# Kernel optimization log

Hardware: AMD Instinct MI355X
Metric: run time of the kernel (lower is better)

The kernel has to match this reference:

```python
import jax, jax.numpy as jnp
import numpy as np

B, T, C = 4, 2048, 768
N_HEAD = 12
HEAD_DIM = C // N_HEAD


def setup_inputs() -> dict:
    key = jax.random.key(0)
    k1, k2, k3 = jax.random.split(key, 3)
    x = jax.random.normal(k1, (B, T, C), dtype=jnp.float32)
    w_attn = jax.random.normal(k2, (C, 3 * C), dtype=jnp.float32) * (1.0 / np.sqrt(C))
    b_attn = jnp.zeros((3 * C,), dtype=jnp.float32)
    w_proj = jax.random.normal(k3, (C, C), dtype=jnp.float32) * (1.0 / np.sqrt(C))
    b_proj = jnp.zeros((C,), dtype=jnp.float32)
    return {"x": x, "w_attn": w_attn, "b_attn": b_attn, "w_proj": w_proj, "b_proj": b_proj}


def reference(x, w_attn, b_attn, w_proj, b_proj):
    # x: [B, T, C]
    Bs, Ts, Cs = x.shape
    qkv = x @ w_attn + b_attn                         # [B, T, 3C]
    q, k, v = jnp.split(qkv, 3, axis=-1)
    # -> [B, H, T, Dh]
    q = q.reshape(Bs, Ts, N_HEAD, HEAD_DIM).swapaxes(1, 2)
    k = k.reshape(Bs, Ts, N_HEAD, HEAD_DIM).swapaxes(1, 2)
    v = v.reshape(Bs, Ts, N_HEAD, HEAD_DIM).swapaxes(1, 2)
    scale = 1.0 / jnp.sqrt(jnp.asarray(HEAD_DIM, dtype=x.dtype))
    att = jnp.einsum('bhqd,bhkd->bhqk', q, k) * scale  # [B, H, T, T]
    causal = jnp.tril(jnp.ones((Ts, Ts), dtype=bool))[None, None]
    att = jnp.where(causal, att, jnp.asarray(-jnp.inf, dtype=att.dtype))
    att = jax.nn.softmax(att, axis=-1)
    y = jnp.einsum('bhqk,bhkd->bhqd', att, v)          # [B, H, T, Dh]
    y = y.swapaxes(1, 2).reshape(Bs, Ts, Cs)
    y = y @ w_proj + b_proj
    return y
```

## Files before the change

kernel.cpp:

```cpp
#include <hip/hip_runtime.h>
#include <cstdint>
#include <cstddef>

typedef __bf16 bf16x8 __attribute__((ext_vector_type(8)));
typedef float  f32x4  __attribute__((ext_vector_type(4)));
typedef unsigned short us;

#define DEV static __device__ __forceinline__

DEV us f2bf(float f) {
    unsigned int u = __builtin_bit_cast(unsigned int, f);
    u += 0x7FFFu + ((u >> 16) & 1u);
    return (us)(u >> 16);
}
DEV unsigned int pack2bf(float a, float b) {
    unsigned int ua = __builtin_bit_cast(unsigned int, a) + 0x8000u;
    unsigned int ub = __builtin_bit_cast(unsigned int, b) + 0x8000u;
    return (ua >> 16) | (ub & 0xFFFF0000u);
}

DEV void gll16(const void* g, void* l) {
    __builtin_amdgcn_global_load_lds(
        (const __attribute__((address_space(1))) unsigned int*)g,
        (__attribute__((address_space(3))) unsigned int*)l, 16, 0, 0);
}

DEV bf16x8 ld_frag(const us* p) {
    return __builtin_bit_cast(bf16x8, *reinterpret_cast<const uint4*>(p));
}

#define BB 4
#define TT 2048
#define CC 768
#define NH 12
#define DH 64
#define MM (BB*TT)
#define QSCALE 0.1803368801111144f

__global__ __launch_bounds__(256)
void cast_k(const float* __restrict__ x, us* __restrict__ xb, int n4)
{
    int i = blockIdx.x * 256 + threadIdx.x;
    int stride = gridDim.x * 256;
    for (; i < n4; i += stride) {
        float4 f = reinterpret_cast<const float4*>(x)[i];
        ushort4 o;
        o.x = f2bf(f.x); o.y = f2bf(f.y); o.z = f2bf(f.z); o.w = f2bf(f.w);
        reinterpret_cast<ushort4*>(xb)[i] = o;
    }
}

__global__ __launch_bounds__(256)
void transpose_k(const float* __restrict__ src,
                 us* __restrict__ dst, int R, int Cc)
{
    __shared__ float tile[32][33];
    int c0 = blockIdx.x * 32, r0 = blockIdx.y * 32;
    int tx = threadIdx.x, ty = threadIdx.y;
#pragma unroll
    for (int i = 0; i < 4; ++i)
        tile[ty + i*8][tx] = src[(size_t)(r0 + ty + i*8) * Cc + c0 + tx];
    __syncthreads();
#pragma unroll
    for (int i = 0; i < 4; ++i)
        dst[(size_t)(c0 + ty + i*8) * R + r0 + tx] = f2bf(tile[tx][ty + i*8]);
}

#define BM 128
#define BN 128
#define BK 32

template<int MODE>
__global__ __launch_bounds__(256)
void gemm_bt(const us* __restrict__ A,
             const us* __restrict__ Bt,
             const float* __restrict__ bias,
             float* __restrict__ Cout,
             us* __restrict__ Qo, us* __restrict__ Ko, us* __restrict__ Vo,
             int M, int N, int K)
{
    __shared__ __align__(16) us As[BM * BK];
    __shared__ __align__(16) us Bs[BN * BK];

    const int tid  = threadIdx.x;
    const int wave = tid >> 6, lane = tid & 63;
    const int quad = lane >> 4, l16 = lane & 15;
    const int waveM = (wave >> 1) * 64, waveN = (wave & 1) * 64;
    const int m0 = blockIdx.y * BM, n0 = blockIdx.x * BN;

    const f32x4 zero4 = {0.f, 0.f, 0.f, 0.f};
    f32x4 acc[4][4];
#pragma unroll
    for (int i = 0; i < 4; ++i)
#pragma unroll
        for (int j = 0; j < 4; ++j) acc[i][j] = zero4;

    const int lrow = lane >> 2, lch = (lane & 3) * 8;
    const int nk = K / BK;
    for (int kt = 0; kt < nk; ++kt) {
#pragma unroll
        for (int c = 0; c < 2; ++c) {
            int rb = (wave * 2 + c) * 16;
            int row = rb + lrow;
            gll16(A  + (size_t)(m0 + row) * K + kt * BK + lch, &As[rb * BK]);
            gll16(Bt + (size_t)(n0 + row) * K + kt * BK + lch, &Bs[rb * BK]);
        }
        __syncthreads();

        bf16x8 af[4], bfv[4];
#pragma unroll
        for (int mi = 0; mi < 4; ++mi)
            af[mi] = *reinterpret_cast<const bf16x8*>(&As[(waveM + mi * 16 + l16) * BK + quad * 8]);
#pragma unroll
        for (int ni = 0; ni < 4; ++ni)
            bfv[ni] = *reinterpret_cast<const bf16x8*>(&Bs[(waveN + ni * 16 + l16) * BK + quad * 8]);
#pragma unroll
        for (int mi = 0; mi < 4; ++mi)
#pragma unroll
            for (int ni = 0; ni < 4; ++ni)
                acc[mi][ni] = __builtin_amdgcn_mfma_f32_16x16x32_bf16(af[mi], bfv[ni], acc[mi][ni], 0, 0, 0);
        __syncthreads();
    }

#pragma unroll
    for (int mi = 0; mi < 4; ++mi) {
#pragma unroll
        for (int ni = 0; ni < 4; ++ni) {
            int n = n0 + waveN + ni * 16 + l16;
            float bv = bias[n];
            int mg = m0 + waveM + mi * 16 + quad * 4;
            if (MODE == 0) {
#pragma unroll
                for (int reg = 0; reg < 4; ++reg)
                    Cout[(size_t)(mg + reg) * N + n] = acc[mi][ni][reg] + bv;
            } else {
                int which = n / CC, c2 = n % CC;
                int h = c2 >> 6, d = c2 & 63;
                int b = mg >> 11, t0 = mg & 2047;
                if (which == 2) {
                    ushort4 pk;
                    pk.x = f2bf(acc[mi][ni][0] + bv);
                    pk.y = f2bf(acc[mi][ni][1] + bv);
                    pk.z = f2bf(acc[mi][ni][2] + bv);
                    pk.w = f2bf(acc[mi][ni][3] + bv);
                    *reinterpret_cast<ushort4*>(Vo + ((size_t)(b * NH + h) * DH + d) * TT + t0) = pk;
                } else {
#pragma unroll
                    for (int reg = 0; reg < 4; ++reg) {
                        size_t off = ((size_t)(b * NH + h) * TT + t0 + reg) * DH + d;
                        float v = acc[mi][ni][reg] + bv;
                        if (which == 0) Qo[off] = f2bf(v * QSCALE);
                        else            Ko[off] = f2bf(v);
                    }
                }
            }
        }
    }
}

#define PST 72

__global__ __launch_bounds__(128)
void attn_k(const us* __restrict__ Qg,
            const us* __restrict__ Kg,
            const us* __restrict__ Vt,
            us* __restrict__ Og)
{
    __shared__ __align__(16) us Ps[2][32 * PST];

    const int tid  = threadIdx.x;
    const int wave = tid >> 6, lane = tid & 63;
    const int quad = lane >> 4, l16 = lane & 15;

    const int id  = blockIdx.x;
    const int xcd = id & 7, s = id >> 3;
    const int bh  = xcd + 8 * (s >> 4);
    const int q   = s & 15;
    const int pw  = 2 * q + wave;

    const size_t base  = (size_t)bh * TT * DH;
    const size_t baseV = (size_t)bh * DH * TT;
    const int b = bh / NH, h = bh % NH;
    us* myP = Ps[wave];

    const f32x4 zero4 = {0.f, 0.f, 0.f, 0.f};

#pragma unroll 1
    for (int seg = 0; seg < 2; ++seg) {
        const int g   = seg ? 63 - pw : pw;
        const int nkt = (g >> 1) + 1;
        const int mA  = g * 32 + l16;
        const int mB  = mA + 16;

        bf16x8 qfA0 = ld_frag(Qg + base + (size_t)mA * DH + quad * 8);
        bf16x8 qfA1 = ld_frag(Qg + base + (size_t)mA * DH + 32 + quad * 8);
        bf16x8 qfB0 = ld_frag(Qg + base + (size_t)mB * DH + quad * 8);
        bf16x8 qfB1 = ld_frag(Qg + base + (size_t)mB * DH + 32 + quad * 8);

        f32x4 oA[4], oB[4];
#pragma unroll
        for (int i = 0; i < 4; ++i) { oA[i] = zero4; oB[i] = zero4; }
        float mrA = -INFINITY, lrA = 0.f, mrB = -INFINITY, lrB = 0.f;

#pragma unroll 1
        for (int j = 0; j < nkt; ++j) {
            const us* kb = Kg + base  + (size_t)j * 64 * DH;
            const us* vb = Vt + baseV + j * 64;

            bf16x8 kf[4][2];
#pragma unroll
            for (int sub = 0; sub < 4; ++sub)
#pragma unroll
                for (int hh = 0; hh < 2; ++hh)
                    kf[sub][hh] = ld_frag(kb + (size_t)(sub * 16 + l16) * DH + hh * 32 + quad * 8);

            f32x4 sA[4], sB[4];
#pragma unroll
            for (int sub = 0; sub < 4; ++sub) {
                f32x4 t = __builtin_amdgcn_mfma_f32_16x16x32_bf16(kf[sub][0], qfA0, zero4, 0, 0, 0);
                sA[sub]  = __builtin_amdgcn_mfma_f32_16x16x32_bf16(kf[sub][1], qfA1, t, 0, 0, 0);
                f32x4 u = __builtin_amdgcn_mfma_f32_16x16x32_bf16(kf[sub][0], qfB0, zero4, 0, 0, 0);
                sB[sub]  = __builtin_amdgcn_mfma_f32_16x16x32_bf16(kf[sub][1], qfB1, u, 0, 0, 0);
            }

            bf16x8 vf[4][2];
#pragma unroll
            for (int dsub = 0; dsub < 4; ++dsub)
#pragma unroll
                for (int kc = 0; kc < 2; ++kc)
                    vf[dsub][kc] = ld_frag(vb + (size_t)(dsub * 16 + l16) * TT + kc * 32 + quad * 8);

            if (j == nkt - 1) {
#pragma unroll
                for (int sub = 0; sub < 4; ++sub)
#pragma unroll
                    for (int reg = 0; reg < 4; ++reg) {
                        int key = j * 64 + sub * 16 + quad * 4 + reg;
                        if (key > mA) sA[sub][reg] = -INFINITY;
                        if (key > mB) sB[sub][reg] = -INFINITY;
                    }
            }

            {
                float mx = -INFINITY;
#pragma unroll
                for (int sub = 0; sub < 4; ++sub)
#pragma unroll
                    for (int reg = 0; reg < 4; ++reg) mx = fmaxf(mx, sA[sub][reg]);
                mx = fmaxf(mx, __shfl_xor(mx, 16));
                mx = fmaxf(mx, __shfl_xor(mx, 32));
                float mnew = fmaxf(mrA, mx);
                float alpha = exp2f(mrA - mnew);
                float rs = 0.f;
#pragma unroll
                for (int sub = 0; sub < 4; ++sub) {
                    float p0 = exp2f(sA[sub][0] - mnew), p1 = exp2f(sA[sub][1] - mnew);
                    float p2 = exp2f(sA[sub][2] - mnew), p3 = exp2f(sA[sub][3] - mnew);
                    rs += (p0 + p1) + (p2 + p3);
                    uint2 pk; pk.x = pack2bf(p0, p1); pk.y = pack2bf(p2, p3);
                    *reinterpret_cast<uint2*>(&myP[l16 * PST + sub * 16 + quad * 4]) = pk;
                }
                rs += __shfl_xor(rs, 16);
                rs += __shfl_xor(rs, 32);
                lrA = lrA * alpha + rs;
                mrA = mnew;
#pragma unroll
                for (int d = 0; d < 4; ++d) oA[d] *= alpha;
            }
            {
                float mx = -INFINITY;
#pragma unroll
                for (int sub = 0; sub < 4; ++sub)
#pragma unroll
                    for (int reg = 0; reg < 4; ++reg) mx = fmaxf(mx, sB[sub][reg]);
                mx = fmaxf(mx, __shfl_xor(mx, 16));
                mx = fmaxf(mx, __shfl_xor(mx, 32));
                float mnew = fmaxf(mrB, mx);
                float alpha = exp2f(mrB - mnew);
                float rs = 0.f;
#pragma unroll
                for (int sub = 0; sub < 4; ++sub) {
                    float p0 = exp2f(sB[sub][0] - mnew), p1 = exp2f(sB[sub][1] - mnew);
                    float p2 = exp2f(sB[sub][2] - mnew), p3 = exp2f(sB[sub][3] - mnew);
                    rs += (p0 + p1) + (p2 + p3);
                    uint2 pk; pk.x = pack2bf(p0, p1); pk.y = pack2bf(p2, p3);
                    *reinterpret_cast<uint2*>(&myP[(16 + l16) * PST + sub * 16 + quad * 4]) = pk;
                }
                rs += __shfl_xor(rs, 16);
                rs += __shfl_xor(rs, 32);
                lrB = lrB * alpha + rs;
                mrB = mnew;
#pragma unroll
                for (int d = 0; d < 4; ++d) oB[d] *= alpha;
            }

#pragma unroll
            for (int kc = 0; kc < 2; ++kc) {
                bf16x8 pfA = *reinterpret_cast<const bf16x8*>(&myP[l16 * PST + kc * 32 + quad * 8]);
                bf16x8 pfB = *reinterpret_cast<const bf16x8*>(&myP[(16 + l16) * PST + kc * 32 + quad * 8]);
#pragma unroll
                for (int d = 0; d < 4; ++d) {
                    oA[d] = __builtin_amdgcn_mfma_f32_16x16x32_bf16(vf[d][kc], pfA, oA[d], 0, 0, 0);
                    oB[d] = __builtin_amdgcn_mfma_f32_16x16x32_bf16(vf[d][kc], pfB, oB[d], 0, 0, 0);
                }
            }
        }

        const float invA = 1.f / lrA, invB = 1.f / lrB;
        us* orowA = Og + ((size_t)(b * TT + mA)) * CC + h * DH;
        us* orowB = Og + ((size_t)(b * TT + mB)) * CC + h * DH;
#pragma unroll
        for (int d = 0; d < 4; ++d) {
            uint2 pa, pb;
            pa.x = pack2bf(oA[d][0] * invA, oA[d][1] * invA);
            pa.y = pack2bf(oA[d][2] * invA, oA[d][3] * invA);
            pb.x = pack2bf(oB[d][0] * invB, oB[d][1] * invB);
            pb.y = pack2bf(oB[d][2] * invB, oB[d][3] * invB);
            *reinterpret_cast<uint2*>(orowA + d * 16 + quad * 4) = pa;
            *reinterpret_cast<uint2*>(orowB + d * 16 + quad * 4) = pb;
        }
    }
}

extern "C" void kernel_launch(void* const* d_in, const int* in_sizes, int n_in,
                              void* d_out, int out_size, void* d_ws, size_t ws_size,
                              hipStream_t stream)
{
    const float* x      = (const float*)d_in[0];
    const float* w_attn = (const float*)d_in[1];
    const float* b_attn = (const float*)d_in[2];
    const float* w_proj = (const float*)d_in[3];
    const float* b_proj = (const float*)d_in[4];
    float* out = (float*)d_out;

    char* ws = (char*)d_ws;
    size_t off = 0;
    auto alloc = [&](size_t bytes) {
        void* p = ws + off;
        off += (bytes + 255) & ~(size_t)255;
        return p;
    };
    us* wtA = (us*)alloc((size_t)(3 * CC) * CC * 2);
    us* wtP = (us*)alloc((size_t)CC * CC * 2);
    us* xb  = (us*)alloc((size_t)MM * CC * 2);
    us* Qb  = (us*)alloc((size_t)MM * CC * 2);
    us* Kb  = (us*)alloc((size_t)MM * CC * 2);
    us* Vtb = (us*)alloc((size_t)MM * CC * 2);
    us* att = (us*)alloc((size_t)MM * CC * 2);

    cast_k<<<1024, 256, 0, stream>>>(x, xb, MM * CC / 4);
    transpose_k<<<dim3((3 * CC) / 32, CC / 32), dim3(32, 8), 0, stream>>>(w_attn, wtA, CC, 3 * CC);
    transpose_k<<<dim3(CC / 32, CC / 32), dim3(32, 8), 0, stream>>>(w_proj, wtP, CC, CC);

    gemm_bt<1><<<dim3((3 * CC) / BN, MM / BM), 256, 0, stream>>>(
        xb, wtA, b_attn, nullptr, Qb, Kb, Vtb, MM, 3 * CC, CC);

    attn_k<<<dim3(16 * BB * NH), 128, 0, stream>>>(Qb, Kb, Vtb, att);

    gemm_bt<0><<<dim3(CC / BN, MM / BM), 256, 0, stream>>>(
        att, wtP, b_proj, out, nullptr, nullptr, nullptr, MM, CC, CC);

    (void)in_sizes; (void)n_in; (void)out_size; (void)ws_size;
}
```

Measured before the change: 263.7 us.

## Stage K/V tiles into double-buffered swizzled LDS shared by both waves

K and V tiles were loaded per wave straight from global memory. Now both waves of a block cooperatively load each 64x64 K and V tile into LDS with async global_load_lds, prefetching the next tile while the current one is used, and read fragments from XOR-swizzled LDS to avoid bank conflicts. Because both waves in a block share a query-tile pair (2q and 2q+1), the key-tile count is unified per block, so the duplicate global traffic is removed. In exchange it adds block-wide barriers each iteration, 32KB of LDS that lowers occupancy, and lockstep between the two waves.

```diff
diff --git a/kernel.cpp b/kernel.cpp
--- a/kernel.cpp
+++ b/kernel.cpp
@@ -160,17 +160,35 @@
 
 #define PST 72
 
+DEV void stage_kv(const us* __restrict__ Kh, const us* __restrict__ Vh, int j,
+                  us* Ks, us* Vs, int wave, int lane)
+{
+    const int rsub = lane >> 3;
+    const int csw  = ((lane & 7) ^ rsub) * 8;
+    const us* kb = Kh + (size_t)j * 64 * DH;
+    const us* vb = Vh + (size_t)j * 64;
+#pragma unroll
+    for (int c = 0; c < 4; ++c) {
+        const int r0 = wave * 32 + c * 8;
+        gll16(kb + (size_t)(r0 + rsub) * DH + csw, Ks + r0 * 64);
+        gll16(vb + (size_t)(r0 + rsub) * TT + csw, Vs + r0 * 64);
+    }
+}
+
 __global__ __launch_bounds__(128)
 void attn_k(const us* __restrict__ Qg,
             const us* __restrict__ Kg,
             const us* __restrict__ Vt,
             us* __restrict__ Og)
 {
+    __shared__ __align__(16) us KsB[2][64 * 64];
+    __shared__ __align__(16) us VsB[2][64 * 64];
     __shared__ __align__(16) us Ps[2][32 * PST];
 
     const int tid  = threadIdx.x;
     const int wave = tid >> 6, lane = tid & 63;
     const int quad = lane >> 4, l16 = lane & 15;
+    const int swz  = l16 & 7;
 
     const int id  = blockIdx.x;
     const int xcd = id & 7, s = id >> 3;
@@ -178,8 +196,9 @@
     const int q   = s & 15;
     const int pw  = 2 * q + wave;
 
-    const size_t base  = (size_t)bh * TT * DH;
-    const size_t baseV = (size_t)bh * DH * TT;
+    const us* Qh = Qg + (size_t)bh * TT * DH;
+    const us* Kh = Kg + (size_t)bh * TT * DH;
+    const us* Vh = Vt + (size_t)bh * DH * TT;
     const int b = bh / NH, h = bh % NH;
     us* myP = Ps[wave];
 
@@ -188,31 +207,38 @@
 #pragma unroll 1
     for (int seg = 0; seg < 2; ++seg) {
         const int g   = seg ? 63 - pw : pw;
-        const int nkt = (g >> 1) + 1;
+        const int nkt = seg ? 32 - q : q + 1;
         const int mA  = g * 32 + l16;
         const int mB  = mA + 16;
 
-        bf16x8 qfA0 = ld_frag(Qg + base + (size_t)mA * DH + quad * 8);
-        bf16x8 qfA1 = ld_frag(Qg + base + (size_t)mA * DH + 32 + quad * 8);
-        bf16x8 qfB0 = ld_frag(Qg + base + (size_t)mB * DH + quad * 8);
-        bf16x8 qfB1 = ld_frag(Qg + base + (size_t)mB * DH + 32 + quad * 8);
+        bf16x8 qfA0 = ld_frag(Qh + (size_t)mA * DH + quad * 8);
+        bf16x8 qfA1 = ld_frag(Qh + (size_t)mA * DH + 32 + quad * 8);
+        bf16x8 qfB0 = ld_frag(Qh + (size_t)mB * DH + quad * 8);
+        bf16x8 qfB1 = ld_frag(Qh + (size_t)mB * DH + 32 + quad * 8);
 
         f32x4 oA[4], oB[4];
 #pragma unroll
         for (int i = 0; i < 4; ++i) { oA[i] = zero4; oB[i] = zero4; }
         float mrA = -INFINITY, lrA = 0.f, mrB = -INFINITY, lrB = 0.f;
 
+        stage_kv(Kh, Vh, 0, KsB[0], VsB[0], wave, lane);
+        __syncthreads();
+        int cur = 0;
+
 #pragma unroll 1
         for (int j = 0; j < nkt; ++j) {
-            const us* kb = Kg + base  + (size_t)j * 64 * DH;
-            const us* vb = Vt + baseV + j * 64;
+            if (j + 1 < nkt)
+                stage_kv(Kh, Vh, j + 1, KsB[cur ^ 1], VsB[cur ^ 1], wave, lane);
+
+            const us* Kt = KsB[cur];
+            const us* Vv = VsB[cur];
 
             bf16x8 kf[4][2];
 #pragma unroll
             for (int sub = 0; sub < 4; ++sub)
 #pragma unroll
                 for (int hh = 0; hh < 2; ++hh)
-                    kf[sub][hh] = ld_frag(kb + (size_t)(sub * 16 + l16) * DH + hh * 32 + quad * 8);
+                    kf[sub][hh] = ld_frag(Kt + (sub * 16 + l16) * 64 + (((hh * 4 + quad) ^ swz) * 8));
 
             f32x4 sA[4], sB[4];
 #pragma unroll
@@ -228,7 +254,7 @@
             for (int dsub = 0; dsub < 4; ++dsub)
 #pragma unroll
                 for (int kc = 0; kc < 2; ++kc)
-                    vf[dsub][kc] = ld_frag(vb + (size_t)(dsub * 16 + l16) * TT + kc * 32 + quad * 8);
+                    vf[dsub][kc] = ld_frag(Vv + (dsub * 16 + l16) * 64 + (((kc * 4 + quad) ^ swz) * 8));
 
             if (j == nkt - 1) {
 #pragma unroll
@@ -304,6 +330,9 @@
                     oB[d] = __builtin_amdgcn_mfma_f32_16x16x32_bf16(vf[d][kc], pfB, oB[d], 0, 0, 0);
                 }
             }
+
+            __syncthreads();
+            cur ^= 1;
         }
 
         const float invA = 1.f / lrA, invB = 1.f / lrB;
```

Result: slower. 297.9 us (+13.0%).
